# Optimization experiments

Hardware: AMD Instinct MI355X
Metric: run time of the kernel (lower is better)

## Reference

```python
import jax, jax.numpy as jnp
import numpy as np

TEMPERATURE = 0.1
NEG_INF = -1e30  # finite sentinel so masked logsumexp has zero (not NaN) gradient


def setup_inputs() -> dict:
    key = jax.random.key(0)
    k1, k2, k3 = jax.random.split(key, 3)
    N, D = 8192, 512          # flattened (batch * TRs) trials, feature dim
    NUM_CLASSES = 3           # vigilance states
    return {
        "objs_feats": jax.random.normal(k1, (N, D), dtype=jnp.float32),
        "objs_labels": jax.random.randint(k2, (N,), 0, NUM_CLASSES, dtype=jnp.int32),
        "bad_tr": jax.random.randint(k3, (N,), 0, 2, dtype=jnp.int32),
    }


def reference(objs_feats, objs_labels, bad_tr):
    # Faithful vectorization of SetCriterion.contrastive_loss_batch_without_break.
    N = objs_feats.shape[0]
    f = objs_feats / jnp.linalg.norm(objs_feats, axis=-1, keepdims=True)
    S = (f @ f.T) / TEMPERATURE                      # [N, N] cosine-sim logits

    valid = bad_tr == 0                              # [N]
    same = objs_labels[:, None] == objs_labels[None, :]
    eye = jnp.eye(N, dtype=bool)
    neg_mask = valid[None, :] & (~same)              # [N, N] negatives per anchor
    pos_mask = valid[None, :] & same & (~eye)        # [N, N] positives per anchor

    has_neg = neg_mask.any(axis=1)
    has_pos = pos_mask.any(axis=1)
    processed = valid & has_neg                      # anchors the loop doesn't `continue` past

    # logsumexp over negatives of each anchor row
    neg_lse = jax.nn.logsumexp(jnp.where(neg_mask, S, NEG_INF), axis=1)  # [N]

    # anchors WITH positives: CE over rows [S[i,p], S[i, negs...]] with target 0,
    # averaged over positives p -> mean_p( logaddexp(S[i,p], neg_lse_i) - S[i,p] )
    ce_per_pos = jnp.logaddexp(S, neg_lse[:, None]) - S                  # [N, N]
    pos_cnt = pos_mask.sum(axis=1)
    loss_with_pos = jnp.where(pos_mask, ce_per_pos, 0.0).sum(axis=1) / jnp.maximum(pos_cnt, 1)

    # anchors WITHOUT positives: pos logit is the constant 1/temperature
    inv_t = jnp.float32(1.0 / TEMPERATURE)
    loss_no_pos = jnp.logaddexp(inv_t, neg_lse) - inv_t

    per_anchor = jnp.where(has_pos, loss_with_pos, loss_no_pos)
    total = jnp.where(processed, per_anchor, 0.0).sum()
    # valid_obj_cnt starts at 1; no-pos anchors net to 0 (−1 then +1)
    count = 1 + (processed & has_pos).sum()
    return total / count.astype(total.dtype)
```

## Files before the change

kernel.cpp:

```cpp
#include <hip/hip_runtime.h>

typedef __bf16 bf16x8 __attribute__((ext_vector_type(8)));
typedef __bf16 bf16x4 __attribute__((ext_vector_type(4)));
typedef float f32x4 __attribute__((ext_vector_type(4)));

#define GLOAD_LDS16(g, l)                                                      \
  __builtin_amdgcn_global_load_lds(                                            \
      (const __attribute__((address_space(1))) void*)(g),                      \
      (__attribute__((address_space(3))) void*)(l), 16, 0, 0)


__global__ __launch_bounds__(1024) void k_scan(
    const int* __restrict__ labels, const int* __restrict__ bad,
    unsigned char* __restrict__ code, int* __restrict__ dst,
    int* __restrict__ hdr, __bf16* __restrict__ fng,
    unsigned char* __restrict__ gcode, float* __restrict__ out, int Nv,
    int Dv) {
  const int t = threadIdx.x;
  const int lane = t & 63, wv = t >> 6;
  const int per = Nv >> 10;
  const int base = t * per;
  unsigned char lc[8];
  int cnt[3] = {0, 0, 0};
  for (int k = 0; k < per; ++k) {
    const int r = base + k;
    const unsigned char c =
        (bad[r] == 0) ? (unsigned char)labels[r] : (unsigned char)255;
    lc[k] = c;
    code[r] = c;
    if (c <= 2) cnt[c]++;
  }
  int inc0 = cnt[0], inc1 = cnt[1], inc2 = cnt[2];
#pragma unroll
  for (int off = 1; off < 64; off <<= 1) {
    const int a = __shfl_up(inc0, off);
    const int b = __shfl_up(inc1, off);
    const int c = __shfl_up(inc2, off);
    if (lane >= off) {
      inc0 += a;
      inc1 += b;
      inc2 += c;
    }
  }
  __shared__ int wt[16][3], wo[17][3];
  if (lane == 63) {
    wt[wv][0] = inc0;
    wt[wv][1] = inc1;
    wt[wv][2] = inc2;
  }
  __syncthreads();
  if (t == 0) {
    int s0 = 0, s1 = 0, s2 = 0;
    for (int w = 0; w < 16; ++w) {
      wo[w][0] = s0;
      wo[w][1] = s1;
      wo[w][2] = s2;
      s0 += wt[w][0];
      s1 += wt[w][1];
      s2 += wt[w][2];
    }
    wo[16][0] = s0;
    wo[16][1] = s1;
    wo[16][2] = s2;
  }
  __syncthreads();
  const int C0 = wo[16][0], C1 = wo[16][1], C2 = wo[16][2];
  int run[3];
  run[0] = wo[wv][0] + inc0 - cnt[0];
  run[1] = C0 + wo[wv][1] + inc1 - cnt[1];
  run[2] = C0 + C1 + wo[wv][2] + inc2 - cnt[2];
  for (int k = 0; k < per; ++k) {
    const int c = lc[k];
    dst[base + k] = (c <= 2) ? run[c]++ : -1;
  }
  const int M = C0 + C1 + C2;
  const int Mpad = (M + 127) & ~127;
  if (t == 0) {
    const int NTv = Mpad >> 7;
    hdr[0] = M;
    hdr[1] = Mpad;
    hdr[2] = NTv;
    hdr[3] = NTv * (NTv + 1) / 2;
    hdr[4] = C0;
    hdr[5] = C1;
    hdr[6] = C2;
    int count = 1;
    if (C0 >= 2 && M > C0) count += C0;
    if (C1 >= 2 && M > C1) count += C1;
    if (C2 >= 2 && M > C2) count += C2;
    hdr[7] = count;
    out[0] = 0.f;
  }
  for (int i = M + t; i < Mpad; i += 1024) gcode[i] = 255;
  const int nv4 = (Mpad - M) * (Dv >> 3);
  float4* fp = (float4*)(fng + (size_t)M * Dv);
  const float4 z = {0.f, 0.f, 0.f, 0.f};
  for (int i = t; i < nv4; i += 1024) fp[i] = z;
}

__global__ __launch_bounds__(512) void k_norm(const float* __restrict__ X,
                                              const unsigned char* __restrict__
                                                  code,
                                              const int* __restrict__ dst,
                                              __bf16* __restrict__ fng,
                                              unsigned char* __restrict__ gcode,
                                              int Nv, int Dv) {
  const int t = threadIdx.x;
  const int tl = t & 63;
  const int row = blockIdx.x * 8 + (t >> 6);
  if (row >= Nv) return;
  const unsigned char c = code[row];
  if (c > 2) return;
  const float4* xr = (const float4*)(X + (size_t)row * Dv);
  if (Dv == 512) {
    const float4 v0 = xr[tl * 2];
    const float4 v1 = xr[tl * 2 + 1];
    float ss = v0.x * v0.x + v0.y * v0.y + v0.z * v0.z + v0.w * v0.w +
               v1.x * v1.x + v1.y * v1.y + v1.z * v1.z + v1.w * v1.w;
#pragma unroll
    for (int off = 1; off < 64; off <<= 1) ss += __shfl_xor(ss, off);
    const float inv = 1.0f / sqrtf(ss);
    const int g = dst[row];
    bf16x8 o;
    o[0] = (__bf16)(v0.x * inv);
    o[1] = (__bf16)(v0.y * inv);
    o[2] = (__bf16)(v0.z * inv);
    o[3] = (__bf16)(v0.w * inv);
    o[4] = (__bf16)(v1.x * inv);
    o[5] = (__bf16)(v1.y * inv);
    o[6] = (__bf16)(v1.z * inv);
    o[7] = (__bf16)(v1.w * inv);
    *(bf16x8*)(fng + (size_t)g * Dv + tl * 8) = o;
    if (tl == 0) gcode[g] = c;
    return;
  }
  float ss = 0.f;
  for (int idx = tl; idx < (Dv >> 2); idx += 64) {
    const float4 v = xr[idx];
    ss += v.x * v.x + v.y * v.y + v.z * v.z + v.w * v.w;
  }
#pragma unroll
  for (int off = 1; off < 64; off <<= 1) ss += __shfl_xor(ss, off);
  const float inv = 1.0f / sqrtf(ss);
  const int g = dst[row];
  for (int idx = tl; idx < (Dv >> 3); idx += 64) {
    const float4 u0 = xr[idx * 2];
    const float4 u1 = xr[idx * 2 + 1];
    bf16x8 o;
    o[0] = (__bf16)(u0.x * inv);
    o[1] = (__bf16)(u0.y * inv);
    o[2] = (__bf16)(u0.z * inv);
    o[3] = (__bf16)(u0.w * inv);
    o[4] = (__bf16)(u1.x * inv);
    o[5] = (__bf16)(u1.y * inv);
    o[6] = (__bf16)(u1.z * inv);
    o[7] = (__bf16)(u1.w * inv);
    *(bf16x8*)(fng + (size_t)g * Dv + idx * 8) = o;
  }
  if (tl == 0) gcode[g] = c;
}

__device__ __forceinline__ void tri_decode(int blk, int NT, int& bi, int& bj) {
  int b = 0, rem = blk, span = NT;
  while (rem >= span) {
    rem -= span;
    b++;
    span--;
  }
  bi = b;
  bj = b + rem;
}

__device__ __forceinline__ int xcd_swz(int w, int n) {
  const int q = n >> 3, r = n & 7, x = w & 7, o = w >> 3;
  return (x < r ? x * (q + 1) : r * (q + 1) + (x - r) * q) + o;
}

__device__ __forceinline__ bool tile_overlap(const unsigned char* gcode,
                                             size_t sA, int lastA,
                                             size_t rowB) {
  const int la0 = gcode[sA], la1 = gcode[sA + lastA];
  const int lb0 = gcode[rowB], lb1 = gcode[rowB + 127];
  const int hiA = la1 > 2 ? 2 : la1;
  const int hiB = lb1 > 2 ? 2 : lb1;
  const int lo = la0 > lb0 ? la0 : lb0;
  const int hi = hiA < hiB ? hiA : hiB;
  return (la0 <= 2) && (lb0 <= 2) && (lo <= hi);
}

__global__ __launch_bounds__(512, 6) void k_p1(
    const __bf16* __restrict__ fng, const unsigned char* __restrict__ gcode,
    const int* __restrict__ hdr, float* __restrict__ P,
    _Float16* __restrict__ Sc, int Nv, int Dv) {
  const int NTv = hdr[2];
  const int ntri = hdr[3];
  int bid = blockIdx.x;
  if (bid >= ntri) return;
  bid = xcd_swz(bid, ntri);
  int bi, bj;
  tri_decode(bid, NTv, bi, bj);
  const size_t sA = (size_t)bi * 128;
  const size_t rowB = (size_t)bj * 128;
  __shared__ __align__(16) __bf16 As[2][128 * 32];
  __shared__ __align__(16) __bf16 Bs[2][128 * 32];

  const int t = threadIdx.x;
  const int lane = t & 63;
  const int wave = t >> 6;
  const int quad = lane >> 4;
  const int l16 = lane & 15;
  const int wr = (wave >> 1) * 32;
  const int wc = (wave & 1) * 64;
  const int r4 = t >> 2, q4 = t & 3;

  f32x4 acc[2][4] = {};
  auto stage = [&](int k0, int b) {
    GLOAD_LDS16(fng + (sA + r4) * Dv + k0 + q4 * 8,
                &As[b][(size_t)wave * 64 * 8]);
    GLOAD_LDS16(fng + (rowB + r4) * Dv + k0 + q4 * 8,
                &Bs[b][(size_t)wave * 64 * 8]);
  };
  stage(0, 0);
  int buf = 0;
  for (int k0 = 0; k0 < Dv; k0 += 32) {
    __syncthreads();
    if (k0 + 32 < Dv) stage(k0 + 32, buf ^ 1);
    bf16x8 af[2], bfv[4];
#pragma unroll
    for (int mi = 0; mi < 2; ++mi)
      af[mi] = *(const bf16x8*)&As[buf][(wr + mi * 16 + l16) * 32 + quad * 8];
#pragma unroll
    for (int ni = 0; ni < 4; ++ni)
      bfv[ni] = *(const bf16x8*)&Bs[buf][(wc + ni * 16 + l16) * 32 + quad * 8];
#pragma unroll
    for (int mi = 0; mi < 2; ++mi)
#pragma unroll
      for (int ni = 0; ni < 4; ++ni)
        acc[mi][ni] = __builtin_amdgcn_mfma_f32_16x16x32_bf16(
            af[mi], bfv[ni], acc[mi][ni], 0, 0, 0);
    buf ^= 1;
  }
  unsigned char ca[8], cb[4];
#pragma unroll
  for (int mi = 0; mi < 2; ++mi)
#pragma unroll
    for (int r = 0; r < 4; ++r)
      ca[mi * 4 + r] = gcode[sA + wr + mi * 16 + quad * 4 + r];
#pragma unroll
  for (int ni = 0; ni < 4; ++ni) cb[ni] = gcode[rowB + wc + ni * 16 + l16];
  const bool ov = tile_overlap(gcode, sA, 127, rowB);
  _Float16* St = Sc + (size_t)bid * 16384;

  float rowsum[8] = {};
  float colsum[4] = {};
#pragma unroll
  for (int mi = 0; mi < 2; ++mi)
#pragma unroll
    for (int ni = 0; ni < 4; ++ni)
#pragma unroll
      for (int r = 0; r < 4; ++r) {
        const float s = acc[mi][ni][r] * 10.0f;
        const float ex = __expf(s);
        const int a = ca[mi * 4 + r], b = cb[ni];
        const bool diff = a != b;
        rowsum[mi * 4 + r] += (b <= 2 && diff) ? ex : 0.f;
        colsum[ni] += (a <= 2 && diff) ? ex : 0.f;
        if (ov)
          St[(wr + mi * 16 + quad * 4 + r) * 128 + wc + ni * 16 + l16] =
              (_Float16)s;
      }
#pragma unroll
  for (int off = 1; off < 16; off <<= 1)
#pragma unroll
    for (int k = 0; k < 8; ++k) rowsum[k] += __shfl_xor(rowsum[k], off);
  if (l16 == 0) {
    const int sreal = bj * 4 + (wave & 1);
    const int szero = bj * 4 + 2 + (wave & 1);
    const size_t r0 = sA + wr + quad * 4;
    float4 v0 = {rowsum[0], rowsum[1], rowsum[2], rowsum[3]};
    float4 v1 = {rowsum[4], rowsum[5], rowsum[6], rowsum[7]};
    const float4 z = {0.f, 0.f, 0.f, 0.f};
    *(float4*)(P + (size_t)sreal * Nv + r0) = v0;
    *(float4*)(P + (size_t)sreal * Nv + r0 + 16) = v1;
    *(float4*)(P + (size_t)szero * Nv + r0) = z;
    *(float4*)(P + (size_t)szero * Nv + r0 + 16) = z;
  }
  if (bi != bj) {
#pragma unroll
    for (int off = 16; off < 64; off <<= 1)
#pragma unroll
      for (int ni = 0; ni < 4; ++ni) colsum[ni] += __shfl_xor(colsum[ni], off);
    if (quad == 0) {
      const int s = bi * 4 + (wave >> 1);
#pragma unroll
      for (int ni = 0; ni < 4; ++ni)
        P[(size_t)s * Nv + rowB + wc + ni * 16 + l16] = colsum[ni];
    }
  }
}

__global__ __launch_bounds__(256) void k_p2(
    const unsigned char* __restrict__ gcode, const int* __restrict__ hdr,
    const float* __restrict__ P, const _Float16* __restrict__ Sc,
    float* __restrict__ out, int Nv) {
  const int NTv = hdr[2];
  const int ntri = hdr[3];
  if ((int)blockIdx.x >= ntri) return;
  const int bid = xcd_swz(blockIdx.x, ntri);
  int bi, bj;
  tri_decode(bid, NTv, bi, bj);
  const size_t sA = (size_t)bi * 128;
  const size_t rowB = (size_t)bj * 128;
  const int t = threadIdx.x;
  const bool diag = (bi == bj);
  if (!tile_overlap(gcode, sA, 127, rowB)) return;

  const int c0 = hdr[4], c1 = hdr[5], c2 = hdr[6];
  const int vt = c0 + c1 + c2;
  __shared__ float E_s[256];
  __shared__ float colpart[128 * 17];
  __shared__ float sd[4];

  {
    const int ns = NTv * 4;
    const size_t g = (t < 128) ? (sA + t) : (rowB + (t - 128));
    float s0 = 0.f, s1 = 0.f, s2 = 0.f, s3 = 0.f;
    int k = 0;
    for (; k + 4 <= ns; k += 4) {
      s0 += P[(size_t)k * Nv + g];
      s1 += P[(size_t)(k + 1) * Nv + g];
      s2 += P[(size_t)(k + 2) * Nv + g];
      s3 += P[(size_t)(k + 3) * Nv + g];
    }
    for (; k < ns; ++k) s0 += P[(size_t)k * Nv + g];
    E_s[t] = (s0 + s1) + (s2 + s3);
  }
  __syncthreads();

  const _Float16* St = Sc + (size_t)bid * 16384;
  const int l8 = t & 15;
  const int rg = t >> 4;
  unsigned char cbv[8];
  float eB[8];
  {
    const uint2 cv = *(const uint2*)(gcode + rowB + l8 * 8);
    const unsigned char* cp = (const unsigned char*)&cv;
#pragma unroll
    for (int e = 0; e < 8; ++e) cbv[e] = cp[e];
#pragma unroll
    for (int e = 0; e < 8; ++e) eB[e] = E_s[128 + l8 * 8 + e];
  }
  float colsum[8] = {};
  float part = 0.f;
#pragma unroll
  for (int k = 0; k < 8; ++k) {
    const int row = k * 16 + rg;
    const int a = gcode[sA + row];
    const float eA = E_s[row];
    const float4 sv = *(const float4*)(St + (size_t)row * 128 + l8 * 8);
    const _Float16* hp = (const _Float16*)&sv;
    float rsum = 0.f;
#pragma unroll
    for (int e = 0; e < 8; ++e) {
      const int col = l8 * 8 + e;
      const float em = __expf(-(float)hp[e]);
      const bool pos =
          (a == cbv[e]) && (cbv[e] <= 2) && !(diag && row == col);
      rsum += pos ? __logf(1.f + eA * em) : 0.f;
      colsum[e] += pos ? __logf(1.f + eB[e] * em) : 0.f;
    }
#pragma unroll
    for (int off = 1; off < 16; off <<= 1) rsum += __shfl_xor(rsum, off);
    if (l8 == 0 && a <= 2) {
      const int cmy = (a == 0) ? c0 : ((a == 1) ? c1 : c2);
      if (vt - cmy > 0 && cmy >= 2) part += rsum / (float)(cmy - 1);
    }
  }
#pragma unroll
  for (int e = 0; e < 8; ++e) colpart[(l8 * 8 + e) * 17 + rg] = colsum[e];
  __syncthreads();
  if (t < 128 && !diag) {
    float cs = 0.f;
#pragma unroll
    for (int i = 0; i < 16; ++i) cs += colpart[t * 17 + i];
    const int b = gcode[rowB + t];
    if (b <= 2) {
      const int cmy = (b == 0) ? c0 : ((b == 1) ? c1 : c2);
      if (vt - cmy > 0 && cmy >= 2) part += cs / (float)(cmy - 1);
    }
  }
  if (diag && t < 128) {
    const int a = gcode[sA + t];
    if (a <= 2) {
      const int cmy = (a == 0) ? c0 : ((a == 1) ? c1 : c2);
      if (vt - cmy > 0 && cmy == 1)
        part += __logf(1.f + E_s[t] * __expf(-10.0f));
    }
  }
#pragma unroll
  for (int off = 32; off; off >>= 1) part += __shfl_down(part, off);
  if ((t & 63) == 0) sd[t >> 6] = part;
  __syncthreads();
  if (t == 0) {
    const float tot = sd[0] + sd[1] + sd[2] + sd[3];
    atomicAdd(out, tot / (float)hdr[7]);
  }
}

extern "C" void kernel_launch(void* const* d_in, const int* in_sizes, int n_in,
                              void* d_out, int out_size, void* d_ws,
                              size_t ws_size, hipStream_t stream) {
  const float* X = (const float*)d_in[0];
  const int* labels = (const int*)d_in[1];
  const int* bad = (const int*)d_in[2];
  const int Nv = in_sizes[1];
  const int Dv = in_sizes[0] / Nv;

  size_t off = 0;
  auto alloc = [&](size_t bytes) -> void* {
    size_t p = (off + 255) & ~(size_t)255;
    off = p + bytes;
    return (void*)((char*)d_ws + p);
  };
  const int NT = Nv / 128;
  const int ntri_max = NT * (NT + 1) / 2;
  __bf16* fng = (__bf16*)alloc((size_t)Nv * Dv * 2);
  float* P = (float*)alloc((size_t)Nv * 256 * 4);
  _Float16* Sc = (_Float16*)alloc((size_t)ntri_max * 16384 * 2);
  int* dst = (int*)alloc((size_t)Nv * 4);
  unsigned char* code = (unsigned char*)alloc((size_t)Nv);
  unsigned char* gcode = (unsigned char*)alloc((size_t)Nv);
  int* hdr = (int*)alloc(64);
  if (off > ws_size) return;
  float* outp = (float*)d_out;

  k_scan<<<1, 1024, 0, stream>>>(labels, bad, code, dst, hdr, fng, gcode,
                                 outp, Nv, Dv);
  k_norm<<<(Nv + 7) / 8, 512, 0, stream>>>(X, code, dst, fng, gcode, Nv, Dv);
  k_p1<<<ntri_max, 512, 0, stream>>>(fng, gcode, hdr, P, Sc, Nv, Dv);
  k_p2<<<ntri_max, 256, 0, stream>>>(gcode, hdr, P, Sc, outp, Nv);
}
```

Baseline: 125.6 us.

## Fuse scan and normalize into one launch; gather rows via index map in GEMM

Merges the label scan and the row normalization into a single kernel. One extra block computes the label-sorted compaction while the other blocks normalize every row in original order. The GEMM now gathers rows through a map array instead of reading a compacted, zero-padded feature buffer. This removes one kernel launch and the serial dependency between scan and normalize. In exchange it normalizes invalid rows too, does indirect row addressing in the GEMM loads, and pads with duplicates of the first valid row instead of zero rows, relying on gcode=255 to mask them.

```diff
diff --git a/kernel.cpp b/kernel.cpp
--- a/kernel.cpp
+++ b/kernel.cpp
@@ -1,7 +1,6 @@
 #include <hip/hip_runtime.h>
 
 typedef __bf16 bf16x8 __attribute__((ext_vector_type(8)));
-typedef __bf16 bf16x4 __attribute__((ext_vector_type(4)));
 typedef float f32x4 __attribute__((ext_vector_type(4)));
 
 #define GLOAD_LDS16(g, l)                                                      \
@@ -10,25 +9,84 @@
       (__attribute__((address_space(3))) void*)(l), 16, 0, 0)
 
 
-__global__ __launch_bounds__(1024) void k_scan(
-    const int* __restrict__ labels, const int* __restrict__ bad,
-    unsigned char* __restrict__ code, int* __restrict__ dst,
-    int* __restrict__ hdr, __bf16* __restrict__ fng,
+__global__ __launch_bounds__(512) void k_prep(
+    const float* __restrict__ X, const int* __restrict__ labels,
+    const int* __restrict__ bad, int* __restrict__ map,
+    int* __restrict__ hdr, __bf16* __restrict__ fn,
     unsigned char* __restrict__ gcode, float* __restrict__ out, int Nv,
-    int Dv) {
+    int Dv, int NB) {
   const int t = threadIdx.x;
+  if ((int)blockIdx.x < NB) {
+    const int tl = t & 63;
+    const int row = blockIdx.x * 8 + (t >> 6);
+    if (row >= Nv) return;
+    const float4* xr = (const float4*)(X + (size_t)row * Dv);
+    if (Dv == 512) {
+      const float4 v0 = xr[tl * 2];
+      const float4 v1 = xr[tl * 2 + 1];
+      float ss = v0.x * v0.x + v0.y * v0.y + v0.z * v0.z + v0.w * v0.w +
+                 v1.x * v1.x + v1.y * v1.y + v1.z * v1.z + v1.w * v1.w;
+#pragma unroll
+      for (int off = 1; off < 64; off <<= 1) ss += __shfl_xor(ss, off);
+      const float inv = 1.0f / sqrtf(ss);
+      bf16x8 o;
+      o[0] = (__bf16)(v0.x * inv);
+      o[1] = (__bf16)(v0.y * inv);
+      o[2] = (__bf16)(v0.z * inv);
+      o[3] = (__bf16)(v0.w * inv);
+      o[4] = (__bf16)(v1.x * inv);
+      o[5] = (__bf16)(v1.y * inv);
+      o[6] = (__bf16)(v1.z * inv);
+      o[7] = (__bf16)(v1.w * inv);
+      *(bf16x8*)(fn + (size_t)row * Dv + tl * 8) = o;
+      return;
+    }
+    float ss = 0.f;
+    for (int idx = tl; idx < (Dv >> 2); idx += 64) {
+      const float4 v = xr[idx];
+      ss += v.x * v.x + v.y * v.y + v.z * v.z + v.w * v.w;
+    }
+#pragma unroll
+    for (int off = 1; off < 64; off <<= 1) ss += __shfl_xor(ss, off);
+    const float inv = 1.0f / sqrtf(ss);
+    for (int idx = tl; idx < (Dv >> 3); idx += 64) {
+      const float4 u0 = xr[idx * 2];
+      const float4 u1 = xr[idx * 2 + 1];
+      bf16x8 o;
+      o[0] = (__bf16)(u0.x * inv);
+      o[1] = (__bf16)(u0.y * inv);
+      o[2] = (__bf16)(u0.z * inv);
+      o[3] = (__bf16)(u0.w * inv);
+      o[4] = (__bf16)(u1.x * inv);
+      o[5] = (__bf16)(u1.y * inv);
+      o[6] = (__bf16)(u1.z * inv);
+      o[7] = (__bf16)(u1.w * inv);
+      *(bf16x8*)(fn + (size_t)row * Dv + idx * 8) = o;
+    }
+    return;
+  }
+
   const int lane = t & 63, wv = t >> 6;
-  const int per = Nv >> 10;
+  const int per = Nv >> 9;
   const int base = t * per;
-  unsigned char lc[8];
+  unsigned char lc[64];
   int cnt[3] = {0, 0, 0};
-  for (int k = 0; k < per; ++k) {
-    const int r = base + k;
-    const unsigned char c =
-        (bad[r] == 0) ? (unsigned char)labels[r] : (unsigned char)255;
-    lc[k] = c;
-    code[r] = c;
-    if (c <= 2) cnt[c]++;
+  {
+    const int4* l4 = (const int4*)(labels + base);
+    const int4* b4 = (const int4*)(bad + base);
+    for (int k = 0; k < (per >> 2); ++k) {
+      const int4 lv = l4[k];
+      const int4 bv = b4[k];
+      const int la[4] = {lv.x, lv.y, lv.z, lv.w};
+      const int ba[4] = {bv.x, bv.y, bv.z, bv.w};
+#pragma unroll
+      for (int e = 0; e < 4; ++e) {
+        const unsigned char c =
+            (ba[e] == 0) ? (unsigned char)la[e] : (unsigned char)255;
+        lc[k * 4 + e] = c;
+        if (c <= 2) cnt[c]++;
+      }
+    }
   }
   int inc0 = cnt[0], inc1 = cnt[1], inc2 = cnt[2];
 #pragma unroll
@@ -42,7 +100,8 @@
       inc2 += c;
     }
   }
-  __shared__ int wt[16][3], wo[17][3];
+  __shared__ int wt[8][3], wo[9][3];
+  __shared__ int first_valid;
   if (lane == 63) {
     wt[wv][0] = inc0;
     wt[wv][1] = inc1;
@@ -51,7 +110,7 @@
   __syncthreads();
   if (t == 0) {
     int s0 = 0, s1 = 0, s2 = 0;
-    for (int w = 0; w < 16; ++w) {
+    for (int w = 0; w < 8; ++w) {
       wo[w][0] = s0;
       wo[w][1] = s1;
       wo[w][2] = s2;
@@ -59,19 +118,24 @@
       s1 += wt[w][1];
       s2 += wt[w][2];
     }
-    wo[16][0] = s0;
-    wo[16][1] = s1;
-    wo[16][2] = s2;
-  }
-  __syncthreads();
-  const int C0 = wo[16][0], C1 = wo[16][1], C2 = wo[16][2];
+    wo[8][0] = s0;
+    wo[8][1] = s1;
+    wo[8][2] = s2;
+  }
+  __syncthreads();
+  const int C0 = wo[8][0], C1 = wo[8][1], C2 = wo[8][2];
   int run[3];
   run[0] = wo[wv][0] + inc0 - cnt[0];
   run[1] = C0 + wo[wv][1] + inc1 - cnt[1];
   run[2] = C0 + C1 + wo[wv][2] + inc2 - cnt[2];
   for (int k = 0; k < per; ++k) {
     const int c = lc[k];
-    dst[base + k] = (c <= 2) ? run[c]++ : -1;
+    if (c <= 2) {
+      const int d = run[c]++;
+      map[d] = base + k;
+      gcode[d] = (unsigned char)c;
+      if (d == 0) first_valid = base + k;
+    }
   }
   const int M = C0 + C1 + C2;
   const int Mpad = (M + 127) & ~127;
@@ -91,73 +155,12 @@
     hdr[7] = count;
     out[0] = 0.f;
   }
-  for (int i = M + t; i < Mpad; i += 1024) gcode[i] = 255;
-  const int nv4 = (Mpad - M) * (Dv >> 3);
-  float4* fp = (float4*)(fng + (size_t)M * Dv);
-  const float4 z = {0.f, 0.f, 0.f, 0.f};
-  for (int i = t; i < nv4; i += 1024) fp[i] = z;
-}
-
-__global__ __launch_bounds__(512) void k_norm(const float* __restrict__ X,
-                                              const unsigned char* __restrict__
-                                                  code,
-                                              const int* __restrict__ dst,
-                                              __bf16* __restrict__ fng,
-                                              unsigned char* __restrict__ gcode,
-                                              int Nv, int Dv) {
-  const int t = threadIdx.x;
-  const int tl = t & 63;
-  const int row = blockIdx.x * 8 + (t >> 6);
-  if (row >= Nv) return;
-  const unsigned char c = code[row];
-  if (c > 2) return;
-  const float4* xr = (const float4*)(X + (size_t)row * Dv);
-  if (Dv == 512) {
-    const float4 v0 = xr[tl * 2];
-    const float4 v1 = xr[tl * 2 + 1];
-    float ss = v0.x * v0.x + v0.y * v0.y + v0.z * v0.z + v0.w * v0.w +
-               v1.x * v1.x + v1.y * v1.y + v1.z * v1.z + v1.w * v1.w;
-#pragma unroll
-    for (int off = 1; off < 64; off <<= 1) ss += __shfl_xor(ss, off);
-    const float inv = 1.0f / sqrtf(ss);
-    const int g = dst[row];
-    bf16x8 o;
-    o[0] = (__bf16)(v0.x * inv);
-    o[1] = (__bf16)(v0.y * inv);
-    o[2] = (__bf16)(v0.z * inv);
-    o[3] = (__bf16)(v0.w * inv);
-    o[4] = (__bf16)(v1.x * inv);
-    o[5] = (__bf16)(v1.y * inv);
-    o[6] = (__bf16)(v1.z * inv);
-    o[7] = (__bf16)(v1.w * inv);
-    *(bf16x8*)(fng + (size_t)g * Dv + tl * 8) = o;
-    if (tl == 0) gcode[g] = c;
-    return;
-  }
-  float ss = 0.f;
-  for (int idx = tl; idx < (Dv >> 2); idx += 64) {
-    const float4 v = xr[idx];
-    ss += v.x * v.x + v.y * v.y + v.z * v.z + v.w * v.w;
-  }
-#pragma unroll
-  for (int off = 1; off < 64; off <<= 1) ss += __shfl_xor(ss, off);
-  const float inv = 1.0f / sqrtf(ss);
-  const int g = dst[row];
-  for (int idx = tl; idx < (Dv >> 3); idx += 64) {
-    const float4 u0 = xr[idx * 2];
-    const float4 u1 = xr[idx * 2 + 1];
-    bf16x8 o;
-    o[0] = (__bf16)(u0.x * inv);
-    o[1] = (__bf16)(u0.y * inv);
-    o[2] = (__bf16)(u0.z * inv);
-    o[3] = (__bf16)(u0.w * inv);
-    o[4] = (__bf16)(u1.x * inv);
-    o[5] = (__bf16)(u1.y * inv);
-    o[6] = (__bf16)(u1.z * inv);
-    o[7] = (__bf16)(u1.w * inv);
-    *(bf16x8*)(fng + (size_t)g * Dv + idx * 8) = o;
-  }
-  if (tl == 0) gcode[g] = c;
+  __syncthreads();
+  const int fv = (M > 0) ? first_valid : 0;
+  for (int i = M + t; i < Mpad; i += 512) {
+    gcode[i] = 255;
+    map[i] = fv;
+  }
 }
 
 __device__ __forceinline__ void tri_decode(int blk, int NT, int& bi, int& bj) {
@@ -189,9 +192,9 @@
 }
 
 __global__ __launch_bounds__(512, 6) void k_p1(
-    const __bf16* __restrict__ fng, const unsigned char* __restrict__ gcode,
-    const int* __restrict__ hdr, float* __restrict__ P,
-    _Float16* __restrict__ Sc, int Nv, int Dv) {
+    const __bf16* __restrict__ fn, const int* __restrict__ map,
+    const unsigned char* __restrict__ gcode, const int* __restrict__ hdr,
+    float* __restrict__ P, _Float16* __restrict__ Sc, int Nv, int Dv) {
   const int NTv = hdr[2];
   const int ntri = hdr[3];
   int bid = blockIdx.x;
@@ -213,12 +216,13 @@
   const int wc = (wave & 1) * 64;
   const int r4 = t >> 2, q4 = t & 3;
 
+  const size_t ma = (size_t)map[sA + r4] * Dv;
+  const size_t mb = (size_t)map[rowB + r4] * Dv;
+
   f32x4 acc[2][4] = {};
   auto stage = [&](int k0, int b) {
-    GLOAD_LDS16(fng + (sA + r4) * Dv + k0 + q4 * 8,
-                &As[b][(size_t)wave * 64 * 8]);
-    GLOAD_LDS16(fng + (rowB + r4) * Dv + k0 + q4 * 8,
-                &Bs[b][(size_t)wave * 64 * 8]);
+    GLOAD_LDS16(fn + ma + k0 + q4 * 8, &As[b][(size_t)wave * 64 * 8]);
+    GLOAD_LDS16(fn + mb + k0 + q4 * 8, &Bs[b][(size_t)wave * 64 * 8]);
   };
   stage(0, 0);
   int buf = 0;
@@ -424,19 +428,18 @@
   };
   const int NT = Nv / 128;
   const int ntri_max = NT * (NT + 1) / 2;
-  __bf16* fng = (__bf16*)alloc((size_t)Nv * Dv * 2);
+  __bf16* fn = (__bf16*)alloc((size_t)Nv * Dv * 2);
   float* P = (float*)alloc((size_t)Nv * 256 * 4);
   _Float16* Sc = (_Float16*)alloc((size_t)ntri_max * 16384 * 2);
-  int* dst = (int*)alloc((size_t)Nv * 4);
-  unsigned char* code = (unsigned char*)alloc((size_t)Nv);
+  int* map = (int*)alloc((size_t)Nv * 4);
   unsigned char* gcode = (unsigned char*)alloc((size_t)Nv);
   int* hdr = (int*)alloc(64);
   if (off > ws_size) return;
   float* outp = (float*)d_out;
 
-  k_scan<<<1, 1024, 0, stream>>>(labels, bad, code, dst, hdr, fng, gcode,
-                                 outp, Nv, Dv);
-  k_norm<<<(Nv + 7) / 8, 512, 0, stream>>>(X, code, dst, fng, gcode, Nv, Dv);
-  k_p1<<<ntri_max, 512, 0, stream>>>(fng, gcode, hdr, P, Sc, Nv, Dv);
+  const int NB = (Nv + 7) / 8;
+  k_prep<<<NB + 1, 512, 0, stream>>>(X, labels, bad, map, hdr, fn, gcode,
+                                     outp, Nv, Dv, NB);
+  k_p1<<<ntri_max, 512, 0, stream>>>(fn, map, gcode, hdr, P, Sc, Nv, Dv);
   k_p2<<<ntri_max, 256, 0, stream>>>(gcode, hdr, P, Sc, outp, Nv);
 }
```

After: 140.1 us. +11.5%, slower.
